# Optimization experiments

Measured on AMD Instinct MI355X. Metric: run time of the kernel, lower is better.

Reference implementation:

```python
import jax, jax.numpy as jnp
import numpy as np

EMB = 256       # hp.emb_dim == hp.hidden_size
MAXN = 512      # hp.max_possible_nodes
B = 128         # number of graphs in batch
N = B * MAXN    # total node rows


def lstm_step(x, h, c, w_ih, w_hh, b_ih, b_hh):
    # torch gate order: i, f, g, o
    gates = x @ w_ih.T + h @ w_hh.T + (b_ih + b_hh)
    i, f, g, o = jnp.split(gates, 4, axis=-1)
    c_new = jax.nn.sigmoid(f) * c + jax.nn.sigmoid(i) * jnp.tanh(g)
    h_new = jax.nn.sigmoid(o) * jnp.tanh(c_new)
    return h_new, c_new


def setup_inputs() -> dict:
    key = jax.random.key(0)
    ks = jax.random.split(key, 12)
    H = EMB
    mu_raw = jax.random.normal(ks[0], (1, N, EMB), jnp.float32)
    batch_col = (jnp.arange(N, dtype=jnp.float32) // MAXN)[None, :, None]
    reach_col = (jax.random.uniform(ks[1], (1, N, 1)) > 0.1).astype(jnp.float32)
    numn_col = jnp.full((1, N, 1), float(MAXN), jnp.float32)
    features = jnp.concatenate([mu_raw, batch_col, reach_col, numn_col], axis=2)
    h0 = jax.random.normal(ks[2], (N, H), jnp.float32) * 0.1
    c0 = jax.random.normal(ks[3], (N, H), jnp.float32) * 0.1
    terminal = jax.random.randint(ks[4], (B,), 0, 2, jnp.int32)
    batch_data = jnp.stack([
        jnp.arange(N, dtype=jnp.int64) // MAXN,
        jnp.zeros((N,), jnp.int64),
        jnp.ones((N,), jnp.int64)], axis=1)
    s = 0.05
    return {
        'features': features, 'h0': h0, 'c0': c0,
        'w_ih': jax.random.normal(ks[5], (4 * H, EMB), jnp.float32) * s,
        'w_hh': jax.random.normal(ks[6], (4 * H, H), jnp.float32) * s,
        'b_ih': jnp.zeros((4 * H,), jnp.float32),
        'b_hh': jnp.zeros((4 * H,), jnp.float32),
        'w5': jax.random.normal(ks[7], (1, 2 * EMB), jnp.float32) * s,
        'b5': jnp.zeros((1,), jnp.float32),
        'w6': jax.random.normal(ks[8], (EMB, EMB), jnp.float32) * s,
        'b6': jnp.zeros((EMB,), jnp.float32),
        'w7': jax.random.normal(ks[9], (EMB, EMB), jnp.float32) * s,
        'b7': jnp.zeros((EMB,), jnp.float32),
        'terminal': terminal, 'batch_data': batch_data,
    }


def reference(features, h0, c0, w_ih, w_hh, b_ih, b_hh, w5, b5, w6, b6, w7, b7, terminal, batch_data):
    # split features: [mu_raw | batch | reachable | num_nodes]
    mu_raw = features[:, :, :EMB]                      # [1, N, EMB]
    batch = features[0, :, EMB].astype(jnp.int32)      # [N] graph ids (sorted blocks)
    reachable = features[0, :, EMB + 1] > 0.5          # [N]

    # zero hidden state for terminal episodes (repeat_interleave by max_nodes)
    term_dense = jnp.repeat(terminal.astype(bool), MAXN)  # [N]
    h0 = jnp.where(term_dense[:, None], 0.0, h0)
    c0 = jnp.where(term_dense[:, None], 0.0, c0)

    # single-layer LSTM over seq (S=1 in this module)
    def step(carry, x):
        h, c = carry
        h, c = lstm_step(x, h, c, w_ih, w_hh, b_ih, b_hh)
        return (h, c), None
    (h, c), _ = jax.lax.scan(step, (h0, c0), mu_raw)
    mu_mem = h                                         # [N, EMB]

    # scatter_mean over graphs
    sums = jax.ops.segment_sum(mu_mem, batch, num_segments=B)
    counts = jax.ops.segment_sum(jnp.ones((N,), mu_mem.dtype), batch, num_segments=B)
    meanpool = sums / counts[:, None]                  # [B, EMB]

    # repeat_interleave back to nodes == gather by batch id (sorted blocks)
    global_state = meanpool[batch] @ w6.T + b6         # [N, EMB]
    local_action = mu_mem @ w7.T + b7                  # [N, EMB]
    rep = jax.nn.relu(jnp.concatenate([global_state, local_action], axis=-1))
    logits = (rep @ w5.T + b5)[:, 0]                   # [N]
    logits = jnp.where(reachable, logits, -jnp.inf)

    # ragged split + pad -> here all graphs are full so this is a reshape
    return logits.reshape(B, MAXN)
```

## Files before the change

kernel.cpp:

```cpp
#include <hip/hip_runtime.h>
#include <math.h>

typedef __attribute__((ext_vector_type(4))) float  f32x4;
typedef __attribute__((ext_vector_type(8))) __bf16 bf16x8;

#define EMB   256
#define FDIM  259
#define MAXN  512
#define NB    128
#define NROWS (NB * MAXN)

#define NEG_SENTINEL (-1e30f)

__device__ __forceinline__ float sigf(float x) { return 1.0f / (1.0f + expf(-x)); }

__device__ __forceinline__ void gll16(const void* g, void* l) {
    __builtin_amdgcn_global_load_lds(
        (const __attribute__((address_space(1))) unsigned int*)g,
        (__attribute__((address_space(3))) unsigned int*)l, 16, 0, 0);
}

#define MFMA(a, b, c) __builtin_amdgcn_mfma_f32_16x16x32_bf16((a), (b), (c), 0, 0, 0)

__global__ __launch_bounds__(256) void k_prep_w(
    const float* __restrict__ w_ih, const float* __restrict__ w_hh,
    const float* __restrict__ w7,
    __bf16* __restrict__ WtA, __bf16* __restrict__ W7t)
{
    const int t = blockIdx.x * 256 + threadIdx.x;
    const float* src;
    __bf16* dh;
    if (t < 65536) {
        const int lane = t & 63, ks = (t >> 6) & 15, db = (t >> 10) & 15, g = t >> 14;
        const int wrow = g * 256 + db * 16 + (lane & 15);
        const int k = (ks & 7) * 32 + (lane >> 4) * 8;
        src = (ks < 8 ? w_ih : w_hh) + (size_t)wrow * 256 + k;
        dh = WtA + (size_t)t * 8;
    } else {
        const int t2 = t - 65536;
        if (t2 >= 8192) return;
        const int lane = t2 & 63, ks = (t2 >> 6) & 7, db = t2 >> 9;
        const int wrow = db * 16 + (lane & 15);
        const int k = ks * 32 + (lane >> 4) * 8;
        src = w7 + (size_t)wrow * 256 + k;
        dh = W7t + (size_t)t2 * 8;
    }
    float4 a = *(const float4*)src, b = *(const float4*)(src + 4);
    float v[8] = {a.x, a.y, a.z, a.w, b.x, b.y, b.z, b.w};
    #pragma unroll
    for (int i = 0; i < 8; i++) dh[i] = (__bf16)v[i];
}

__global__ __launch_bounds__(512, 2) void k_lstm_mfma(
    const float* __restrict__ feat, const float* __restrict__ h0,
    const float* __restrict__ c0,
    const float* __restrict__ b_ih, const float* __restrict__ b_hh,
    const int* __restrict__ terminal,
    const __bf16* __restrict__ WtA,
    __bf16* __restrict__ H)
{
    __shared__ __align__(16) __bf16 As[4096];
    __shared__ __align__(16) __bf16 Bs[16384];

    const int bid = blockIdx.x;
    const int m0 = (bid >> 1) * 128, D0 = (bid & 1) * 128;
    const int tid = threadIdx.x, w = tid >> 6, l = tid & 63;
    const int wr = w >> 2, wc = w & 3;
    const bool term = terminal[m0 >> 9] != 0;

    f32x4 acc[4][2][4];
    #pragma unroll
    for (int rf = 0; rf < 4; rf++)
        #pragma unroll
        for (int dg = 0; dg < 2; dg++)
            #pragma unroll
            for (int g = 0; g < 4; g++)
                acc[rf][dg][g] = (f32x4){0.f, 0.f, 0.f, 0.f};

    const int skg = (tid >> 4) & 3, srw = tid & 15;
    const int srow = m0 + (tid >> 6) * 16 + srw;

    for (int ks = 0; ks < 16; ++ks) {
        const int k0 = ks * 32;
        __syncthreads();
        float v[8];
        if (ks < 8) {
            const float* p = feat + (size_t)srow * FDIM + k0 + skg * 8;
            #pragma unroll
            for (int i = 0; i < 8; i++) v[i] = p[i];
        } else if (term) {
            #pragma unroll
            for (int i = 0; i < 8; i++) v[i] = 0.f;
        } else {
            const float* p = h0 + (size_t)srow * 256 + (k0 - 256) + skg * 8;
            float4 a = *(const float4*)p, b = *(const float4*)(p + 4);
            v[0] = a.x; v[1] = a.y; v[2] = a.z; v[3] = a.w;
            v[4] = b.x; v[5] = b.y; v[6] = b.z; v[7] = b.w;
        }
        bf16x8 hv;
        #pragma unroll
        for (int i = 0; i < 8; i++) hv[i] = (__bf16)v[i];
        *(bf16x8*)&As[tid * 8] = hv;
        #pragma unroll
        for (int i = 0; i < 4; i++) {
            const int ct = w * 4 + i;
            const int g = ct >> 3, dbl = ct & 7;
            const size_t off = ((size_t)((g * 16 + (D0 >> 4) + dbl) * 16 + ks) * 64 + l) * 8;
            gll16(WtA + off, &Bs[ct * 512]);
        }
        __syncthreads();
        bf16x8 ah[4];
        #pragma unroll
        for (int rf = 0; rf < 4; rf++)
            ah[rf] = *(const bf16x8*)&As[((wr * 4 + rf) * 64 + l) * 8];
        #pragma unroll
        for (int dg = 0; dg < 2; dg++) {
            const int ctb = wc * 2 + dg;
            bf16x8 bh[4];
            #pragma unroll
            for (int g = 0; g < 4; g++)
                bh[g] = *(const bf16x8*)&Bs[((g * 8 + ctb) * 64 + l) * 8];
            #pragma unroll
            for (int rf = 0; rf < 4; rf++)
                #pragma unroll
                for (int g = 0; g < 4; g++)
                    acc[rf][dg][g] = MFMA(ah[rf], bh[g], acc[rf][dg][g]);
        }
    }

    #pragma unroll
    for (int rf = 0; rf < 4; rf++)
        #pragma unroll
        for (int dg = 0; dg < 2; dg++) {
            const int dim = D0 + wc * 32 + dg * 16 + (l & 15);
            float bias[4];
            #pragma unroll
            for (int g = 0; g < 4; g++)
                bias[g] = b_ih[g * 256 + dim] + b_hh[g * 256 + dim];
            #pragma unroll
            for (int r = 0; r < 4; r++) {
                const int row = m0 + wr * 64 + rf * 16 + (l >> 4) * 4 + r;
                const float gi = acc[rf][dg][0][r] + bias[0];
                const float gf = acc[rf][dg][1][r] + bias[1];
                const float gg = acc[rf][dg][2][r] + bias[2];
                const float go = acc[rf][dg][3][r] + bias[3];
                const float c0v = term ? 0.f : c0[(size_t)row * 256 + dim];
                const float cn = sigf(gf) * c0v + sigf(gi) * tanhf(gg);
                const float hn = sigf(go) * tanhf(cn);
                H[(size_t)row * 256 + dim] = (__bf16)hn;
            }
        }
}

__global__ __launch_bounds__(256) void k_meanpool(
    const __bf16* __restrict__ H, float* __restrict__ mpp)
{
    __shared__ float red[8][256];
    const int b = blockIdx.x, seg = blockIdx.y, t = threadIdx.x;
    const int rg = t >> 5, cg = t & 31;
    float s[8];
    #pragma unroll
    for (int j = 0; j < 8; j++) s[j] = 0.f;
    const size_t base = ((size_t)b * MAXN + seg * 64 + rg * 8) * 256 + cg * 8;
    #pragma unroll
    for (int r = 0; r < 8; r++) {
        bf16x8 vh = *(const bf16x8*)(H + base + (size_t)r * 256);
        #pragma unroll
        for (int j = 0; j < 8; j++) s[j] += (float)vh[j];
    }
    #pragma unroll
    for (int j = 0; j < 8; j++) red[rg][cg * 8 + j] = s[j];
    __syncthreads();
    float tot = 0.f;
    #pragma unroll
    for (int g = 0; g < 8; g++) tot += red[g][t];
    mpp[((size_t)seg * NB + b) * 256 + t] = tot;
}

__global__ __launch_bounds__(256) void k_gdot(
    const float* __restrict__ mpp, const float* __restrict__ w6,
    const float* __restrict__ b6, const float* __restrict__ w5,
    const float* __restrict__ b5, float* __restrict__ gdot)
{
    __shared__ float smp[256];
    __shared__ float red[256];
    const int b = blockIdx.x, j = threadIdx.x;
    float m = 0.f;
    #pragma unroll
    for (int p = 0; p < 8; p++) m += mpp[((size_t)p * NB + b) * 256 + j];
    smp[j] = m * (1.0f / MAXN);
    __syncthreads();
    const float* wr = w6 + (size_t)j * 256;
    float s = b6[j];
    #pragma unroll 4
    for (int k = 0; k < 256; k++) s = fmaf(smp[k], wr[k], s);
    red[j] = fmaxf(s, 0.f) * w5[j];
    __syncthreads();
    for (int off = 128; off > 0; off >>= 1) {
        if (j < off) red[j] += red[j + off];
        __syncthreads();
    }
    if (j == 0) gdot[b] = red[0] + b5[0];
}

__global__ __launch_bounds__(256, 2) void k_final_mfma(
    const __bf16* __restrict__ H, const __bf16* __restrict__ W7t,
    const float* __restrict__ b7, const float* __restrict__ w5,
    const float* __restrict__ feat, const float* __restrict__ gdot,
    float* __restrict__ out)
{
    __shared__ __align__(16) __bf16 As[4096];
    __shared__ __align__(16) __bf16 Bs[8192];

    const int m0 = blockIdx.x * 128;
    const int tid = threadIdx.x, w = tid >> 6, l = tid & 63;

    f32x4 acc[2][16];
    #pragma unroll
    for (int rf = 0; rf < 2; rf++)
        #pragma unroll
        for (int ct = 0; ct < 16; ct++)
            acc[rf][ct] = (f32x4){0.f, 0.f, 0.f, 0.f};

    for (int ks = 0; ks < 8; ++ks) {
        const int k0 = ks * 32;
        __syncthreads();
        #pragma unroll
        for (int cc = 0; cc < 2; cc++) {
            const int c = tid + cc * 256;
            const int rf = c >> 6, kg = (c >> 4) & 3, row = c & 15;
            const size_t src = (size_t)(m0 + rf * 16 + row) * 256 + k0 + kg * 8;
            gll16(H + src, &As[(cc * 256 + w * 64) * 8]);
        }
        #pragma unroll
        for (int i = 0; i < 4; i++) {
            const int ct = w * 4 + i;
            const size_t off = ((size_t)(ct * 8 + ks) * 64 + l) * 8;
            gll16(W7t + off, &Bs[ct * 512]);
        }
        __syncthreads();
        bf16x8 ah[2];
        #pragma unroll
        for (int rf = 0; rf < 2; rf++)
            ah[rf] = *(const bf16x8*)&As[((w * 2 + rf) * 64 + l) * 8];
        #pragma unroll
        for (int ct = 0; ct < 16; ct++) {
            bf16x8 bh = *(const bf16x8*)&Bs[(ct * 64 + l) * 8];
            #pragma unroll
            for (int rf = 0; rf < 2; rf++)
                acc[rf][ct] = MFMA(ah[rf], bh, acc[rf][ct]);
        }
    }

    const int cl = l & 15;
    float part[2][4];
    #pragma unroll
    for (int rf = 0; rf < 2; rf++)
        #pragma unroll
        for (int r = 0; r < 4; r++) part[rf][r] = 0.f;
    #pragma unroll
    for (int ct = 0; ct < 16; ct++) {
        const int col = ct * 16 + cl;
        const float b7v = b7[col], w5v = w5[256 + col];
        #pragma unroll
        for (int rf = 0; rf < 2; rf++)
            #pragma unroll
            for (int r = 0; r < 4; r++)
                part[rf][r] += fmaxf(acc[rf][ct][r] + b7v, 0.f) * w5v;
    }
    #pragma unroll
    for (int rf = 0; rf < 2; rf++)
        #pragma unroll
        for (int r = 0; r < 4; r++) {
            float s = part[rf][r];
            s += __shfl_xor(s, 1, 64);
            s += __shfl_xor(s, 2, 64);
            s += __shfl_xor(s, 4, 64);
            s += __shfl_xor(s, 8, 64);
            part[rf][r] = s;
        }
    if (cl == 0) {
        #pragma unroll
        for (int rf = 0; rf < 2; rf++)
            #pragma unroll
            for (int r = 0; r < 4; r++) {
                const int row = m0 + w * 32 + rf * 16 + (l >> 4) * 4 + r;
                const float logit = part[rf][r] + gdot[row >> 9];
                const bool reach = feat[(size_t)row * FDIM + 257] > 0.5f;
                out[row] = reach ? logit : NEG_SENTINEL;
            }
    }
}

extern "C" void kernel_launch(void* const* d_in, const int* in_sizes, int n_in,
                              void* d_out, int out_size, void* d_ws, size_t ws_size,
                              hipStream_t stream)
{
    const float* feat     = (const float*)d_in[0];
    const float* h0       = (const float*)d_in[1];
    const float* c0       = (const float*)d_in[2];
    const float* w_ih     = (const float*)d_in[3];
    const float* w_hh     = (const float*)d_in[4];
    const float* b_ih     = (const float*)d_in[5];
    const float* b_hh     = (const float*)d_in[6];
    const float* w5       = (const float*)d_in[7];
    const float* b5       = (const float*)d_in[8];
    const float* w6       = (const float*)d_in[9];
    const float* b6       = (const float*)d_in[10];
    const float* w7       = (const float*)d_in[11];
    const float* b7       = (const float*)d_in[12];
    const int*   terminal = (const int*)d_in[13];

    float* out = (float*)d_out;
    char*  ws  = (char*)d_ws;
    __bf16* H    = (__bf16*)(ws);
    __bf16* WtA  = (__bf16*)(ws + 33554432);
    __bf16* W7t  = (__bf16*)(ws + 34603008);
    float*  mpp  = (float*)(ws + 34734080);
    float*  gd   = (float*)(ws + 35782656);

    k_prep_w<<<288, 256, 0, stream>>>(w_ih, w_hh, w7, WtA, W7t);
    k_lstm_mfma<<<1024, 512, 0, stream>>>(feat, h0, c0, b_ih, b_hh,
                                          terminal, WtA, H);
    k_meanpool<<<dim3(NB, 8), 256, 0, stream>>>(H, mpp);
    k_gdot<<<NB, 256, 0, stream>>>(mpp, w6, b6, w5, b5, gd);
    k_final_mfma<<<512, 256, 0, stream>>>(H, W7t, b7, w5, feat, gd, out);
}
```

Measured before the change: 402.4 us.

## Double-buffer LDS tiles in LSTM and final GEMM kernels to overlap loads

Both MFMA GEMM kernels now use two LDS buffers for the A and B tiles. Each k-step issues the next step's global loads (direct-to-LDS for the weights, registers then convert for the features and h0) before running the current step's MFMAs, which cuts one barrier per iteration. The aim is to hide global memory latency behind matrix compute. In exchange LDS use per block doubles (about 80KB in the LSTM kernel), which may limit the 2-blocks-per-CU occupancy that launch_bounds asks for, and live register pressure goes up.

New measurement: 389.4 us. 1.03x faster.

```diff
diff --git a/kernel.cpp b/kernel.cpp
--- a/kernel.cpp
+++ b/kernel.cpp
@@ -59,8 +59,8 @@
     const __bf16* __restrict__ WtA,
     __bf16* __restrict__ H)
 {
-    __shared__ __align__(16) __bf16 As[4096];
-    __shared__ __align__(16) __bf16 Bs[16384];
+    __shared__ __align__(16) __bf16 As[2][4096];
+    __shared__ __align__(16) __bf16 Bs[2][16384];
 
     const int bid = blockIdx.x;
     const int m0 = (bid >> 1) * 128, D0 = (bid & 1) * 128;
@@ -77,55 +77,77 @@
             for (int g = 0; g < 4; g++)
                 acc[rf][dg][g] = (f32x4){0.f, 0.f, 0.f, 0.f};
 
-    const int skg = (tid >> 4) & 3, srw = tid & 15;
-    const int srow = m0 + (tid >> 6) * 16 + srw;
-
-    for (int ks = 0; ks < 16; ++ks) {
-        const int k0 = ks * 32;
-        __syncthreads();
+    const int skg = (tid >> 4) & 3;
+    const int srow = m0 + (tid >> 6) * 16 + (tid & 15);
+    const float* featp = feat + (size_t)srow * FDIM + skg * 8;
+    const float* h0p   = h0   + (size_t)srow * 256 + skg * 8;
+
+    {
         float v[8];
-        if (ks < 8) {
-            const float* p = feat + (size_t)srow * FDIM + k0 + skg * 8;
-            #pragma unroll
-            for (int i = 0; i < 8; i++) v[i] = p[i];
-        } else if (term) {
-            #pragma unroll
-            for (int i = 0; i < 8; i++) v[i] = 0.f;
-        } else {
-            const float* p = h0 + (size_t)srow * 256 + (k0 - 256) + skg * 8;
-            float4 a = *(const float4*)p, b = *(const float4*)(p + 4);
-            v[0] = a.x; v[1] = a.y; v[2] = a.z; v[3] = a.w;
-            v[4] = b.x; v[5] = b.y; v[6] = b.z; v[7] = b.w;
-        }
+        __builtin_memcpy(v, featp, 32);
         bf16x8 hv;
         #pragma unroll
         for (int i = 0; i < 8; i++) hv[i] = (__bf16)v[i];
-        *(bf16x8*)&As[tid * 8] = hv;
+        *(bf16x8*)&As[0][tid * 8] = hv;
         #pragma unroll
         for (int i = 0; i < 4; i++) {
             const int ct = w * 4 + i;
             const int g = ct >> 3, dbl = ct & 7;
-            const size_t off = ((size_t)((g * 16 + (D0 >> 4) + dbl) * 16 + ks) * 64 + l) * 8;
-            gll16(WtA + off, &Bs[ct * 512]);
-        }
-        __syncthreads();
+            const size_t off = ((size_t)((g * 16 + (D0 >> 4) + dbl) * 16 + 0) * 64 + l) * 8;
+            gll16(WtA + off, &Bs[0][ct * 512]);
+        }
+    }
+    __syncthreads();
+
+    int cur = 0;
+    for (int ks = 0; ks < 16; ++ks) {
+        const bool st = (ks < 15);
+        const int nb = cur ^ 1, ksn = ks + 1;
+        float v[8];
+        if (st) {
+            if (ksn < 8) {
+                __builtin_memcpy(v, featp + ksn * 32, 32);
+            } else if (term) {
+                #pragma unroll
+                for (int i = 0; i < 8; i++) v[i] = 0.f;
+            } else {
+                __builtin_memcpy(v, h0p + (ksn - 8) * 32, 32);
+            }
+            #pragma unroll
+            for (int i = 0; i < 4; i++) {
+                const int ct = w * 4 + i;
+                const int g = ct >> 3, dbl = ct & 7;
+                const size_t off = ((size_t)((g * 16 + (D0 >> 4) + dbl) * 16 + ksn) * 64 + l) * 8;
+                gll16(WtA + off, &Bs[nb][ct * 512]);
+            }
+        }
         bf16x8 ah[4];
         #pragma unroll
         for (int rf = 0; rf < 4; rf++)
-            ah[rf] = *(const bf16x8*)&As[((wr * 4 + rf) * 64 + l) * 8];
+            ah[rf] = *(const bf16x8*)&As[cur][((wr * 4 + rf) * 64 + l) * 8];
+        bf16x8 bh[2][4];
         #pragma unroll
         for (int dg = 0; dg < 2; dg++) {
             const int ctb = wc * 2 + dg;
-            bf16x8 bh[4];
             #pragma unroll
             for (int g = 0; g < 4; g++)
-                bh[g] = *(const bf16x8*)&Bs[((g * 8 + ctb) * 64 + l) * 8];
+                bh[dg][g] = *(const bf16x8*)&Bs[cur][((g * 8 + ctb) * 64 + l) * 8];
+        }
+        if (st) {
+            bf16x8 hv;
+            #pragma unroll
+            for (int i = 0; i < 8; i++) hv[i] = (__bf16)v[i];
+            *(bf16x8*)&As[nb][tid * 8] = hv;
+        }
+        #pragma unroll
+        for (int dg = 0; dg < 2; dg++)
             #pragma unroll
             for (int rf = 0; rf < 4; rf++)
                 #pragma unroll
                 for (int g = 0; g < 4; g++)
-                    acc[rf][dg][g] = MFMA(ah[rf], bh[g], acc[rf][dg][g]);
-        }
+                    acc[rf][dg][g] = MFMA(ah[rf], bh[dg][g], acc[rf][dg][g]);
+        __syncthreads();
+        cur ^= 1;
     }
 
     #pragma unroll
@@ -209,8 +231,8 @@
     const float* __restrict__ feat, const float* __restrict__ gdot,
     float* __restrict__ out)
 {
-    __shared__ __align__(16) __bf16 As[4096];
-    __shared__ __align__(16) __bf16 Bs[8192];
+    __shared__ __align__(16) __bf16 As[2][4096];
+    __shared__ __align__(16) __bf16 Bs[2][8192];
 
     const int m0 = blockIdx.x * 128;
     const int tid = threadIdx.x, w = tid >> 6, l = tid & 63;
@@ -222,34 +244,53 @@
         for (int ct = 0; ct < 16; ct++)
             acc[rf][ct] = (f32x4){0.f, 0.f, 0.f, 0.f};
 
+    #pragma unroll
+    for (int cc = 0; cc < 2; cc++) {
+        const int c = tid + cc * 256;
+        const int rf = c >> 6, kg = (c >> 4) & 3, row = c & 15;
+        const size_t src = (size_t)(m0 + rf * 16 + row) * 256 + kg * 8;
+        gll16(H + src, &As[0][(cc * 256 + w * 64) * 8]);
+    }
+    #pragma unroll
+    for (int i = 0; i < 4; i++) {
+        const int ct = w * 4 + i;
+        const size_t off = ((size_t)(ct * 8 + 0) * 64 + l) * 8;
+        gll16(W7t + off, &Bs[0][ct * 512]);
+    }
+    __syncthreads();
+
+    int cur = 0;
     for (int ks = 0; ks < 8; ++ks) {
-        const int k0 = ks * 32;
-        __syncthreads();
-        #pragma unroll
-        for (int cc = 0; cc < 2; cc++) {
-            const int c = tid + cc * 256;
-            const int rf = c >> 6, kg = (c >> 4) & 3, row = c & 15;
-            const size_t src = (size_t)(m0 + rf * 16 + row) * 256 + k0 + kg * 8;
-            gll16(H + src, &As[(cc * 256 + w * 64) * 8]);
-        }
-        #pragma unroll
-        for (int i = 0; i < 4; i++) {
-            const int ct = w * 4 + i;
-            const size_t off = ((size_t)(ct * 8 + ks) * 64 + l) * 8;
-            gll16(W7t + off, &Bs[ct * 512]);
-        }
-        __syncthreads();
+        const int nb = cur ^ 1, ksn = ks + 1;
+        if (ks < 7) {
+            const int k0n = ksn * 32;
+            #pragma unroll
+            for (int cc = 0; cc < 2; cc++) {
+                const int c = tid + cc * 256;
+                const int rf = c >> 6, kg = (c >> 4) & 3, row = c & 15;
+                const size_t src = (size_t)(m0 + rf * 16 + row) * 256 + k0n + kg * 8;
+                gll16(H + src, &As[nb][(cc * 256 + w * 64) * 8]);
+            }
+            #pragma unroll
+            for (int i = 0; i < 4; i++) {
+                const int ct = w * 4 + i;
+                const size_t off = ((size_t)(ct * 8 + ksn) * 64 + l) * 8;
+                gll16(W7t + off, &Bs[nb][ct * 512]);
+            }
+        }
         bf16x8 ah[2];
         #pragma unroll
         for (int rf = 0; rf < 2; rf++)
-            ah[rf] = *(const bf16x8*)&As[((w * 2 + rf) * 64 + l) * 8];
+            ah[rf] = *(const bf16x8*)&As[cur][((w * 2 + rf) * 64 + l) * 8];
         #pragma unroll
         for (int ct = 0; ct < 16; ct++) {
-            bf16x8 bh = *(const bf16x8*)&Bs[(ct * 64 + l) * 8];
+            bf16x8 bh = *(const bf16x8*)&Bs[cur][(ct * 64 + l) * 8];
             #pragma unroll
             for (int rf = 0; rf < 2; rf++)
                 acc[rf][ct] = MFMA(ah[rf], bh, acc[rf][ct]);
         }
+        __syncthreads();
+        cur ^= 1;
     }
 
     const int cl = l & 15;
```
